# Kernel tuning notes

Hardware: AMD Instinct MI355X
Metric: run time of the kernel (lower is better)

Reference implementation:

```python
import jax, jax.numpy as jnp
import numpy as np

K = 7            # kernel_size
PAD = K // 2
B, C, H, W = 16, 4, 128, 128   # in_channels == out_channels == 4


def setup_inputs() -> dict:
    key = jax.random.key(0)
    kx, kw = jax.random.split(key)
    x = jax.random.normal(kx, (B, C, H, W), dtype=jnp.float32)
    # nn.Parameter init: randn * 0.0001 / kernel_size
    weight = jax.random.normal(kw, (1, C, C, H, W, K * K), dtype=jnp.float32) * (0.0001 / K)
    return {"x": x, "weight": weight}


def reference(x, weight):
    # fmri mask computed on the (possibly) pre-padded input
    mask = (x != 0).astype(x.dtype)                       # (B,C,H,W)
    xp = jnp.pad(x, ((0, 0), (0, 0), (PAD, PAD), (PAD, PAD)))
    # unfold(2,K,1).unfold(3,K,1).view(..., K*K): taps ordered row-major (dy, dx)
    patches = jnp.stack(
        [xp[:, :, dy:dy + H, dx:dx + W] for dy in range(K) for dx in range(K)],
        axis=-1,
    )                                                      # (B,C,H,W,K*K)
    # weight_bias: delta kernel (1 at the center tap)
    wb = jnp.zeros((1, C, C, H, W, K * K), dtype=x.dtype).at[..., (K * K) // 2].set(1.0)
    cw = weight + wb
    # L1-normalized absolute weights over the tap dimension
    wn = jnp.abs(cw) / jnp.sum(jnp.abs(cw), axis=-1, keepdims=True)
    # out[b,o,h,w] = sum_{i,t} patches[b,i,h,w,t] * wn[0,o,i,h,w,t]
    out = jnp.einsum('bihwt,oihwt->bohw', patches, wn[0])
    return out * mask
```

## Files before the change

kernel.cpp:

```cpp
#include <hip/hip_runtime.h>


typedef float fvec4 __attribute__((ext_vector_type(4)));
typedef float fvec2 __attribute__((ext_vector_type(2)));

#define HW 128
#define PW 134
#define NC 4
#define KK 49
#define WC 8
#define RP 52
#define XTP_FLOATS (NC * PW * PW * 16)

__global__ __launch_bounds__(256) void lc2d_prep(const float* __restrict__ x,
                                                 float* __restrict__ xTp) {
  int idx = blockIdx.x * 256 + threadIdx.x;
  if (idx >= NC * PW * PW) return;
  int wp = idx % PW;
  int r  = idx / PW;
  int hp = r % PW;
  int i  = r / PW;
  int h = hp - 3, w = wp - 3;
  bool in = (h >= 0) & (h < HW) & (w >= 0) & (w < HW);
  float v[16];
#pragma unroll
  for (int b = 0; b < 16; ++b)
    v[b] = in ? x[((b * NC + i) * HW + h) * HW + w] : 0.0f;
  float4* dst = (float4*)(xTp + (size_t)idx * 16);
  dst[0] = make_float4(v[0],  v[1],  v[2],  v[3]);
  dst[1] = make_float4(v[4],  v[5],  v[6],  v[7]);
  dst[2] = make_float4(v[8],  v[9],  v[10], v[11]);
  dst[3] = make_float4(v[12], v[13], v[14], v[15]);
}

__global__ __launch_bounds__(64)
void lc2d_fused5(const float* __restrict__ weight,
                 const float* __restrict__ xTp,
                 float* __restrict__ out) {
  __shared__ __align__(16) float Wl[16][WC][RP];

  const int tid = threadIdx.x;
  const int bid = blockIdx.x;
  const int wc  = bid >> 7;
  const int h   = bid & 127;
  const int w0  = wc * WC;

  const float* wb = weight + (size_t)(h * HW + w0) * KK;
#pragma unroll
  for (int k = 0; k < 25; ++k) {
    int f = tid + k * 64;
    if (f < 1568) {
      int oi = f / 98;
      int fl = f - oi * 98;
      fvec4 v = *(const fvec4*)(wb + (size_t)oi * 802816 + 4 * fl);
      int e = 4 * fl;
#pragma unroll
      for (int j = 0; j < 4; ++j) {
        int ee = e + j;
        int p  = ee / 49;
        int t  = ee - p * 49;
        Wl[oi][p][t] = v[j];
      }
    }
  }
  __syncthreads();

  const int bp  = tid & 7;
  const int pos = tid >> 3;

  fvec2 acc0 = {0.f, 0.f}, acc1 = acc0, acc2 = acc0, acc3 = acc0;

  for (int i = 0; i < NC; ++i) {
    const float* xb = xTp + ((size_t)(i * PW + h) * PW + (w0 + pos)) * 16 + 2 * bp;
    fvec2 t0 = {0.f, 0.f}, t1 = t0, t2 = t0, t3 = t0;
    float s0 = 0.f, s1 = 0.f, s2 = 0.f, s3 = 0.f;
#pragma unroll
    for (int tg = 0; tg < 12; ++tg) {
      fvec4 q0 = *(const fvec4*)&Wl[0 * 4 + i][pos][tg * 4];
      fvec4 q1 = *(const fvec4*)&Wl[1 * 4 + i][pos][tg * 4];
      fvec4 q2 = *(const fvec4*)&Wl[2 * 4 + i][pos][tg * 4];
      fvec4 q3 = *(const fvec4*)&Wl[3 * 4 + i][pos][tg * 4];
#pragma unroll
      for (int j = 0; j < 4; ++j) {
        const int t  = tg * 4 + j;
        const int dy = t / 7, dx = t - dy * 7;
        fvec2 xv = *(const fvec2*)(xb + (dy * PW + dx) * 16);
        float wa = q0[j], wbv = q1[j], wcv = q2[j], wd = q3[j];
        if (t == 24) { wa += 1.f; wbv += 1.f; wcv += 1.f; wd += 1.f; }
        float a0 = fabsf(wa), a1 = fabsf(wbv), a2 = fabsf(wcv), a3 = fabsf(wd);
        s0 += a0; s1 += a1; s2 += a2; s3 += a3;
        t0 += xv * a0; t1 += xv * a1; t2 += xv * a2; t3 += xv * a3;
      }
    }
    {
      fvec2 xv = *(const fvec2*)(xb + (6 * PW + 6) * 16);
      float a0 = fabsf(Wl[0 * 4 + i][pos][48]);
      float a1 = fabsf(Wl[1 * 4 + i][pos][48]);
      float a2 = fabsf(Wl[2 * 4 + i][pos][48]);
      float a3 = fabsf(Wl[3 * 4 + i][pos][48]);
      s0 += a0; s1 += a1; s2 += a2; s3 += a3;
      t0 += xv * a0; t1 += xv * a1; t2 += xv * a2; t3 += xv * a3;
    }
    acc0 += t0 * (1.f / s0);
    acc1 += t1 * (1.f / s1);
    acc2 += t2 * (1.f / s2);
    acc3 += t3 * (1.f / s3);
  }

  const int obase = h * HW + w0 + pos;
#pragma unroll
  for (int o = 0; o < NC; ++o) {
    fvec2 m = *(const fvec2*)(xTp +
        ((size_t)(o * PW + h + 3) * PW + (w0 + pos + 3)) * 16 + 2 * bp);
    fvec2 a = (o == 0) ? acc0 : (o == 1) ? acc1 : (o == 2) ? acc2 : acc3;
    out[(size_t)((2 * bp + 0) * NC + o) * 16384 + obase] = (m[0] != 0.f) ? a[0] : 0.f;
    out[(size_t)((2 * bp + 1) * NC + o) * 16384 + obase] = (m[1] != 0.f) ? a[1] : 0.f;
  }
}

__global__ __launch_bounds__(256) void lc2d_nows(const float* __restrict__ weight,
                                                 const float* __restrict__ x,
                                                 float* __restrict__ out) {
  __shared__ __align__(16) float Raw[NC * 784];
  const int tid = threadIdx.x;
  const int bid = blockIdx.x;
  const int i   = bid >> 10;
  const int r2  = bid & 1023;
  const int h   = r2 >> 3;
  const int wcc = r2 & 7;
  const int w0  = wcc * 16;
  const size_t wbase = (size_t)i * 802816 + (size_t)(h * HW + w0) * KK;
#pragma unroll
  for (int k = 0; k < 4; ++k) {
    int f = tid + k * 256;
    if (f < 784) {
      int o = f / 196, g = f - o * 196;
      *(float4*)(&Raw[o * 784 + 4 * g]) =
          *(const float4*)(weight + wbase + (size_t)o * 3211264 + 4 * g);
    }
  }
  __syncthreads();
  {
    const int r = tid >> 2, q = tid & 3;
    const int rowb = (r >> 4) * 784 + (r & 15) * KK;
    const int t0 = q * 12;
    float v[13];
#pragma unroll
    for (int j = 0; j < 12; ++j) v[j] = Raw[rowb + t0 + j];
    v[12] = (q == 3) ? Raw[rowb + 48] : 0.f;
    float s = 0.f;
#pragma unroll
    for (int j = 0; j < 13; ++j) s += fabsf(v[j]);
    if (q == 2) s += fabsf(v[0] + 1.f) - fabsf(v[0]);
    s += __shfl_xor(s, 1);
    s += __shfl_xor(s, 2);
    const float inv = 1.f / s;
    if (q == 2) v[0] += 1.f;
#pragma unroll
    for (int j = 0; j < 12; ++j) Raw[rowb + t0 + j] = fabsf(v[j]) * inv;
    if (q == 3) Raw[rowb + 48] = fabsf(v[12]) * inv;
  }
  __syncthreads();
  const int b = tid & 15, pos = tid >> 4, w = w0 + pos;
  float acc[NC] = {0.f, 0.f, 0.f, 0.f};
  float xv[7];
#pragma unroll
  for (int dy = 0; dy < 7; ++dy) {
    int hh = h + dy - 3;
    bool hin = (hh >= 0) & (hh < HW);
#pragma unroll
    for (int dx = 0; dx < 7; ++dx) {
      int ww = w + dx - 3;
      bool in = hin & (ww >= 0) & (ww < HW);
      xv[dx] = in ? x[((b * NC + i) * HW + hh) * HW + ww] : 0.f;
    }
#pragma unroll
    for (int o = 0; o < NC; ++o) {
      const float* wr = &Raw[o * 784 + pos * KK + dy * 7];
#pragma unroll
      for (int dx = 0; dx < 7; ++dx) acc[o] = fmaf(xv[dx], wr[dx], acc[o]);
    }
  }
#pragma unroll
  for (int o = 0; o < NC; ++o) {
    float xc = x[((b * NC + o) * HW + h) * HW + w];
    atomicAdd(&out[((b * NC + o) * HW + h) * HW + w], (xc != 0.f) ? acc[o] : 0.f);
  }
}

extern "C" void kernel_launch(void* const* d_in, const int* in_sizes, int n_in,
                              void* d_out, int out_size, void* d_ws, size_t ws_size,
                              hipStream_t stream) {
  const float* x      = (const float*)d_in[0];
  const float* weight = (const float*)d_in[1];
  float* out = (float*)d_out;

  const size_t xtp_bytes = (size_t)XTP_FLOATS * 4;
  if (ws_size >= xtp_bytes) {
    float* xTp = (float*)d_ws;
    lc2d_prep<<<(NC * PW * PW + 255) / 256, 256, 0, stream>>>(x, xTp);
    lc2d_fused5<<<2048, 64, 0, stream>>>(weight, xTp, out);
  } else {
    hipMemsetAsync(d_out, 0, (size_t)out_size * sizeof(float), stream);
    lc2d_nows<<<4096, 256, 0, stream>>>(weight, x, out);
  }
}
```

Before: 121.7 us.

## Split input-channel loop across four wavefronts with shared-memory reduction

The fused kernel now uses 256 threads per block instead of 64, with each wavefront handling one input channel rather than one thread looping over all four. Partial sums per output channel are reduced through shared memory (reusing the weight tile buffer, padded by 9 floats per lane), and each wavefront then writes one output channel. This raises parallelism and latency hiding for the weight load and the gather loop, at the cost of two extra barriers and a small LDS reduction.

New measurement: 175.8 us. +44.4%, slower.

```diff
diff --git a/kernel.cpp b/kernel.cpp
--- a/kernel.cpp
+++ b/kernel.cpp
@@ -33,22 +33,26 @@
   dst[3] = make_float4(v[12], v[13], v[14], v[15]);
 }
 
-__global__ __launch_bounds__(64)
-void lc2d_fused5(const float* __restrict__ weight,
+__global__ __launch_bounds__(256, 4)
+void lc2d_fused7(const float* __restrict__ weight,
                  const float* __restrict__ xTp,
                  float* __restrict__ out) {
   __shared__ __align__(16) float Wl[16][WC][RP];
 
-  const int tid = threadIdx.x;
-  const int bid = blockIdx.x;
-  const int wc  = bid >> 7;
-  const int h   = bid & 127;
-  const int w0  = wc * WC;
+  const int tid  = threadIdx.x;
+  const int wv   = tid >> 6;
+  const int lane = tid & 63;
+  const int pos  = lane >> 3;
+  const int bp   = lane & 7;
+  const int bid  = blockIdx.x;
+  const int wc   = bid >> 7;
+  const int h    = bid & 127;
+  const int w0   = wc * WC;
 
   const float* wb = weight + (size_t)(h * HW + w0) * KK;
 #pragma unroll
-  for (int k = 0; k < 25; ++k) {
-    int f = tid + k * 64;
+  for (int k = 0; k < 7; ++k) {
+    int f = tid + k * 256;
     if (f < 1568) {
       int oi = f / 98;
       int fl = f - oi * 98;
@@ -65,57 +69,61 @@
   }
   __syncthreads();
 
-  const int bp  = tid & 7;
-  const int pos = tid >> 3;
-
-  fvec2 acc0 = {0.f, 0.f}, acc1 = acc0, acc2 = acc0, acc3 = acc0;
-
-  for (int i = 0; i < NC; ++i) {
-    const float* xb = xTp + ((size_t)(i * PW + h) * PW + (w0 + pos)) * 16 + 2 * bp;
-    fvec2 t0 = {0.f, 0.f}, t1 = t0, t2 = t0, t3 = t0;
-    float s0 = 0.f, s1 = 0.f, s2 = 0.f, s3 = 0.f;
-#pragma unroll
-    for (int tg = 0; tg < 12; ++tg) {
-      fvec4 q0 = *(const fvec4*)&Wl[0 * 4 + i][pos][tg * 4];
-      fvec4 q1 = *(const fvec4*)&Wl[1 * 4 + i][pos][tg * 4];
-      fvec4 q2 = *(const fvec4*)&Wl[2 * 4 + i][pos][tg * 4];
-      fvec4 q3 = *(const fvec4*)&Wl[3 * 4 + i][pos][tg * 4];
-#pragma unroll
-      for (int j = 0; j < 4; ++j) {
-        const int t  = tg * 4 + j;
-        const int dy = t / 7, dx = t - dy * 7;
-        fvec2 xv = *(const fvec2*)(xb + (dy * PW + dx) * 16);
-        float wa = q0[j], wbv = q1[j], wcv = q2[j], wd = q3[j];
-        if (t == 24) { wa += 1.f; wbv += 1.f; wcv += 1.f; wd += 1.f; }
-        float a0 = fabsf(wa), a1 = fabsf(wbv), a2 = fabsf(wcv), a3 = fabsf(wd);
-        s0 += a0; s1 += a1; s2 += a2; s3 += a3;
-        t0 += xv * a0; t1 += xv * a1; t2 += xv * a2; t3 += xv * a3;
-      }
-    }
-    {
-      fvec2 xv = *(const fvec2*)(xb + (6 * PW + 6) * 16);
-      float a0 = fabsf(Wl[0 * 4 + i][pos][48]);
-      float a1 = fabsf(Wl[1 * 4 + i][pos][48]);
-      float a2 = fabsf(Wl[2 * 4 + i][pos][48]);
-      float a3 = fabsf(Wl[3 * 4 + i][pos][48]);
+  const int i = wv;
+  const float* xb = xTp + ((size_t)(i * PW + h) * PW + (w0 + pos)) * 16 + 2 * bp;
+
+  float s0 = 0.f, s1 = 0.f, s2 = 0.f, s3 = 0.f;
+  fvec2 t0 = {0.f, 0.f}, t1 = t0, t2 = t0, t3 = t0;
+
+#pragma unroll
+  for (int tg = 0; tg < 12; ++tg) {
+    fvec4 q0 = *(const fvec4*)&Wl[0 * 4 + i][pos][tg * 4];
+    fvec4 q1 = *(const fvec4*)&Wl[1 * 4 + i][pos][tg * 4];
+    fvec4 q2 = *(const fvec4*)&Wl[2 * 4 + i][pos][tg * 4];
+    fvec4 q3 = *(const fvec4*)&Wl[3 * 4 + i][pos][tg * 4];
+#pragma unroll
+    for (int j = 0; j < 4; ++j) {
+      const int t  = tg * 4 + j;
+      const int dy = t / 7, dx = t - dy * 7;
+      fvec2 xv = *(const fvec2*)(xb + (dy * PW + dx) * 16);
+      float a0 = q0[j], a1 = q1[j], a2 = q2[j], a3 = q3[j];
+      if (t == 24) { a0 += 1.f; a1 += 1.f; a2 += 1.f; a3 += 1.f; }
+      a0 = fabsf(a0); a1 = fabsf(a1); a2 = fabsf(a2); a3 = fabsf(a3);
       s0 += a0; s1 += a1; s2 += a2; s3 += a3;
       t0 += xv * a0; t1 += xv * a1; t2 += xv * a2; t3 += xv * a3;
     }
-    acc0 += t0 * (1.f / s0);
-    acc1 += t1 * (1.f / s1);
-    acc2 += t2 * (1.f / s2);
-    acc3 += t3 * (1.f / s3);
-  }
-
-  const int obase = h * HW + w0 + pos;
-#pragma unroll
-  for (int o = 0; o < NC; ++o) {
-    fvec2 m = *(const fvec2*)(xTp +
-        ((size_t)(o * PW + h + 3) * PW + (w0 + pos + 3)) * 16 + 2 * bp);
-    fvec2 a = (o == 0) ? acc0 : (o == 1) ? acc1 : (o == 2) ? acc2 : acc3;
-    out[(size_t)((2 * bp + 0) * NC + o) * 16384 + obase] = (m[0] != 0.f) ? a[0] : 0.f;
-    out[(size_t)((2 * bp + 1) * NC + o) * 16384 + obase] = (m[1] != 0.f) ? a[1] : 0.f;
-  }
+  }
+  {
+    fvec2 xv = *(const fvec2*)(xb + (6 * PW + 6) * 16);
+    float a0 = fabsf(Wl[0 * 4 + i][pos][48]);
+    float a1 = fabsf(Wl[1 * 4 + i][pos][48]);
+    float a2 = fabsf(Wl[2 * 4 + i][pos][48]);
+    float a3 = fabsf(Wl[3 * 4 + i][pos][48]);
+    s0 += a0; s1 += a1; s2 += a2; s3 += a3;
+    t0 += xv * a0; t1 += xv * a1; t2 += xv * a2; t3 += xv * a3;
+  }
+  t0 *= (1.f / s0); t1 *= (1.f / s1); t2 *= (1.f / s2); t3 *= (1.f / s3);
+
+  __syncthreads();
+  float* Red = (float*)Wl;
+  float* rp = Red + (wv * 64 + lane) * 9;
+  rp[0] = t0[0]; rp[1] = t0[1]; rp[2] = t1[0]; rp[3] = t1[1];
+  rp[4] = t2[0]; rp[5] = t2[1]; rp[6] = t3[0]; rp[7] = t3[1];
+  __syncthreads();
+
+  const int o = wv;
+  float r0 = 0.f, r1 = 0.f;
+#pragma unroll
+  for (int k = 0; k < 4; ++k) {
+    const float* q = Red + (k * 64 + lane) * 9 + o * 2;
+    r0 += q[0];
+    r1 += q[1];
+  }
+  fvec2 m = *(const fvec2*)(xTp +
+      ((size_t)(o * PW + h + 3) * PW + (w0 + pos + 3)) * 16 + 2 * bp);
+  const size_t ob = (size_t)h * HW + w0 + pos;
+  out[(size_t)((2 * bp + 0) * NC + o) * 16384 + ob] = (m[0] != 0.f) ? r0 : 0.f;
+  out[(size_t)((2 * bp + 1) * NC + o) * 16384 + ob] = (m[1] != 0.f) ? r1 : 0.f;
 }
 
 __global__ __launch_bounds__(256) void lc2d_nows(const float* __restrict__ weight,
@@ -199,7 +207,7 @@
   if (ws_size >= xtp_bytes) {
     float* xTp = (float*)d_ws;
     lc2d_prep<<<(NC * PW * PW + 255) / 256, 256, 0, stream>>>(x, xTp);
-    lc2d_fused5<<<2048, 64, 0, stream>>>(weight, xTp, out);
+    lc2d_fused7<<<2048, 256, 0, stream>>>(weight, xTp, out);
   } else {
     hipMemsetAsync(d_out, 0, (size_t)out_size * sizeof(float), stream);
     lc2d_nows<<<4096, 256, 0, stream>>>(weight, x, out);
```
